# Optimization experiments

Measured on AMD Instinct MI355X. Metric: run time of the kernel, lower is better.

Reference implementation:

```python
import jax, jax.numpy as jnp
import numpy as np

D_MODEL = 768
N_HEAD = 12


def setup_inputs() -> dict:
    key = jax.random.key(0)
    k1, k2, k3, k4, k5 = jax.random.split(key, 5)
    B, T, C = 4, 2048, D_MODEL
    s = 1.0 / np.sqrt(C)
    return {
        "x": jax.random.normal(k1, (B, T, C), dtype=jnp.float32),
        "w_attn": jax.random.normal(k2, (C, 3 * C), dtype=jnp.float32) * s,
        "b_attn": jax.random.normal(k3, (3 * C,), dtype=jnp.float32) * 0.02,
        "w_proj": jax.random.normal(k4, (C, C), dtype=jnp.float32) * s,
        "b_proj": jax.random.normal(k5, (C,), dtype=jnp.float32) * 0.02,
    }


def reference(x, w_attn, b_attn, w_proj, b_proj):
    B, T, C = x.shape
    H = N_HEAD
    Dh = C // H
    qkv = x @ w_attn + b_attn                      # [B, T, 3C]
    q, k, v = jnp.split(qkv, 3, axis=-1)
    # [B, H, T, Dh]
    q = q.reshape(B, T, H, Dh).transpose(0, 2, 1, 3)
    k = k.reshape(B, T, H, Dh).transpose(0, 2, 1, 3)
    v = v.reshape(B, T, H, Dh).transpose(0, 2, 1, 3)
    att = jnp.einsum("bhqd,bhkd->bhqk", q, k) * (1.0 / np.sqrt(Dh))
    causal = jnp.tril(jnp.ones((T, T), dtype=bool))
    att = jnp.where(causal[None, None, :, :], att, -jnp.inf)
    att = jax.nn.softmax(att, axis=-1)             # dropout p=0 (eval)
    y = jnp.einsum("bhqk,bhkd->bhqd", att, v)      # [B, H, T, Dh]
    y = y.transpose(0, 2, 1, 3).reshape(B, T, C)
    return y @ w_proj + b_proj
```

## Files before the change

### kernel.cpp

```cpp
#include <hip/hip_runtime.h>
#include <stdint.h>

#define NHEAD 12
#define DH 64
#define BATCH 4
#define SEQ 2048
#define CDIM 768
#define MROWS (BATCH*SEQ)

typedef __attribute__((ext_vector_type(8))) short short8;
typedef __attribute__((ext_vector_type(4))) float floatx4;
typedef unsigned int u32;

__device__ inline unsigned short f2bf(float f) {
    union { float f; unsigned u; } v; v.f = f;
    unsigned r = v.u + 0x7FFFu + ((v.u >> 16) & 1u);
    return (unsigned short)(r >> 16);
}

__device__ __forceinline__ u32 pk_bf16(float a, float b) {
    u32 d;
    asm("v_cvt_pk_bf16_f32 %0, %1, %2" : "=v"(d) : "v"(a), "v"(b));
    return d;
}

__device__ __forceinline__ void async_cp16(const unsigned short* g, unsigned short* l) {
    __builtin_amdgcn_global_load_lds(
        (const __attribute__((address_space(1))) u32*)g,
        (__attribute__((address_space(3))) u32*)l, 16, 0, 0);
}

template<int N> __device__ __forceinline__ void waitcnt_vm() {
    if constexpr (N == 0)      asm volatile("s_waitcnt vmcnt(0)" ::: "memory");
    else if constexpr (N == 3) asm volatile("s_waitcnt vmcnt(3)" ::: "memory");
    else if constexpr (N == 4) asm volatile("s_waitcnt vmcnt(4)" ::: "memory");
}

__device__ __forceinline__ void transpose_tile(
    const float* __restrict__ in, unsigned short* __restrict__ out,
    int K, int N, int k0, int n0, unsigned short (*T)[72]) {
    const int t = threadIdx.x;
    const int nc = t & 63, kw = t >> 6;
    for (int i = 0; i < 16; i++) {
        const int kr = kw + i * 4;
        T[nc][kr] = f2bf(in[(size_t)(k0 + kr) * N + n0 + nc]);
    }
    __syncthreads();
    const int row = t >> 2, seg = t & 3;
    uint4 a = *(const uint4*)&T[row][seg * 16];
    uint4 b2 = *(const uint4*)&T[row][seg * 16 + 8];
    unsigned short* o = &out[(size_t)(n0 + row) * K + k0 + seg * 16];
    *(uint4*)o = a;
    *(uint4*)(o + 8) = b2;
}

__global__ __launch_bounds__(256) void prep_kernel(
    const float* __restrict__ x,      unsigned short* __restrict__ xb,
    const float* __restrict__ wa,     unsigned short* __restrict__ wta,
    const float* __restrict__ wp,     unsigned short* __restrict__ wtp) {
    __shared__ unsigned short T[64][72];
    const int lin = blockIdx.x;
    if (lin < 6144) {
        const int i = (lin * 256 + threadIdx.x) * 4;
        float4 f = *(const float4*)(x + i);
        union { unsigned short s[4]; uint2 u; } p;
        p.s[0] = f2bf(f.x); p.s[1] = f2bf(f.y);
        p.s[2] = f2bf(f.z); p.s[3] = f2bf(f.w);
        *(uint2*)(xb + i) = p.u;
    } else if (lin < 6144 + 432) {
        const int t2 = lin - 6144;
        transpose_tile(wa, wta, CDIM, 3 * CDIM, (t2 % 12) * 64, (t2 / 12) * 64, T);
    } else {
        const int t3 = lin - 6576;
        transpose_tile(wp, wtp, CDIM, CDIM, (t3 % 12) * 64, (t3 / 12) * 64, T);
    }
}

template<int MODE, int KD, int BM, int BN>
__global__ __launch_bounds__(256) void gemm_bf16(
    const unsigned short* __restrict__ A,
    const unsigned short* __restrict__ BT,
    const float* __restrict__ bias,
    float* __restrict__ Cout,
    unsigned short* __restrict__ Qout,
    unsigned short* __restrict__ Kout,
    unsigned short* __restrict__ VTout,
    int Ndim)
{
    constexpr int TM = BM / 32, TN = BN / 32;
    constexpr int CHA = BM / 64, CHB = BN / 64;
    __shared__ unsigned short SH[3 * (BM + BN) * 32];
    auto As = [&](int b3) { return &SH[b3 * BM * 32]; };
    auto Bs = [&](int b3) { return &SH[3 * BM * 32 + b3 * BN * 32]; };

    const int tid  = threadIdx.x;
    const int wave = tid >> 6;
    const int lane = tid & 63;
    const int l16  = lane & 15;
    const int quad = lane >> 4;
    const int wm = wave >> 1, wn = wave & 1;
    const int m0 = blockIdx.x * BM;
    const int n0 = blockIdx.y * BN;

    const int rloc = lane >> 2;
    const int gs   = (((lane & 3) ^ (rloc & 3) ^ ((rloc >> 2) & 3))) * 8;
    const int pg   = ((quad ^ (l16 & 3) ^ ((l16 >> 2) & 3))) * 8;

    floatx4 acc[TM][TN];
    for (int i = 0; i < TM; i++)
        for (int j = 0; j < TN; j++) acc[i][j] = (floatx4)0.0f;

    constexpr int NIT = KD / 32;

    auto stageTo = [&](int s, int buf) {
        const int koff = s * 32;
        for (int ch = 0; ch < CHA; ch++) {
            const int row = wave * CHA * 16 + ch * 16 + rloc;
            async_cp16(&A[(size_t)(m0 + row) * KD + koff + gs],
                       &As(buf)[(wave * CHA + ch) * 512]);
        }
        for (int ch = 0; ch < CHB; ch++) {
            const int row = wave * CHB * 16 + ch * 16 + rloc;
            async_cp16(&BT[(size_t)(n0 + row) * KD + koff + gs],
                       &Bs(buf)[(wave * CHB + ch) * 512]);
        }
    };
    stageTo(0, 0);
    stageTo(1, 1);

    int buf = 0;
    for (int it = 0; it < NIT; it++) {
        if (it < NIT - 1) waitcnt_vm<CHA + CHB>();
        else              waitcnt_vm<0>();
        asm volatile("s_barrier" ::: "memory");
        if (it + 2 < NIT) {
            int b2 = buf + 2; if (b2 >= 3) b2 -= 3;
            stageTo(it + 2, b2);
        }
        short8 a[TM], b[TN];
        for (int i = 0; i < TM; i++)
            a[i] = *(const short8*)&As(buf)[(wm * (BM / 2) + i * 16 + l16) * 32 + pg];
        for (int j = 0; j < TN; j++)
            b[j] = *(const short8*)&Bs(buf)[(wn * (BN / 2) + j * 16 + l16) * 32 + pg];
        for (int i = 0; i < TM; i++)
            for (int j = 0; j < TN; j++)
                acc[i][j] = __builtin_amdgcn_mfma_f32_16x16x32_bf16(
                    a[i], b[j], acc[i][j], 0, 0, 0);
        buf++; if (buf >= 3) buf = 0;
    }

    const float QSCALE = 0.18033688011112042f;

    if (MODE == 1 && (n0 / CDIM) == 2) {
        __syncthreads();
        unsigned short* scr = &SH[wave * (64 * 68)];
        for (int i = 0; i < TM; i++) {
            const int tl = i * 16 + quad * 4;
            for (int j = 0; j < TN; j++) {
                const int dl = j * 16 + l16;
                const float bv = bias[n0 + wn * 64 + j * 16 + l16];
                uint2 u;
                u.x = pk_bf16(acc[i][j][0] + bv, acc[i][j][1] + bv);
                u.y = pk_bf16(acc[i][j][2] + bv, acc[i][j][3] + bv);
                *(uint2*)&scr[dl * 68 + tl] = u;
            }
        }
        const int b_ = m0 >> 11;
        const int tg = (m0 & 2047) + wm * 64;
        const int h  = (n0 - 2 * CDIM + wn * 64) >> 6;
        const size_t rowbase = ((size_t)(b_ * NHEAD + h)) * DH;
        for (int p = 0; p < 8; p++) {
            const int d  = p * 8 + (lane >> 3);
            const int tc = (lane & 7) * 8;
            uint4 v = *(const uint4*)&scr[d * 68 + tc];
            *(uint4*)&VTout[(rowbase + d) * SEQ + tg + tc] = v;
        }
        return;
    }

    for (int i = 0; i < TM; i++) {
        const int mbase = m0 + wm * (BM / 2) + i * 16 + quad * 4;
        for (int j = 0; j < TN; j++) {
            const int ncj  = n0 + wn * (BN / 2) + j * 16;
            const int ncol = ncj + l16;
            const float bv = bias[ncol];
            for (int r = 0; r < 4; r++) {
                const int m = mbase + r;
                const float v = acc[i][j][r] + bv;
                if (MODE == 0) {
                    Cout[(size_t)m * Ndim + ncol] = v;
                } else {
                    const int part = ncj / CDIM;
                    const int c = ncol - part * CDIM;
                    const int hh = c >> 6, d = c & 63;
                    const int b_ = m >> 11, t = m & 2047;
                    const size_t bh = (size_t)(b_ * NHEAD + hh);
                    if (part == 0)
                        Qout[(bh * SEQ + t) * DH + d] = f2bf(v * QSCALE);
                    else
                        Kout[(bh * SEQ + t) * DH + d] = f2bf(v);
                }
            }
        }
    }
}

__global__ __launch_bounds__(256) void attn_kernel(
    const unsigned short* __restrict__ Q,
    const unsigned short* __restrict__ K,
    const unsigned short* __restrict__ VT,
    unsigned short* __restrict__ O)
{
    __shared__ unsigned short Kl[2][2][64 * 32];
    __shared__ unsigned short Vl[2][2][64 * 32];
    __shared__ unsigned short Pl[4][16 * 68];

    const int tid  = threadIdx.x;
    const int wave = tid >> 6;
    const int lane = tid & 63;
    const int l16  = lane & 15;
    const int quad = lane >> 4;

    const int lin = blockIdx.x;
    const int grp = lin >> 3;
    const int xs  = grp & 15;
    const int bh  = ((grp >> 4) << 3) | (lin & 7);
    const int h = bh % NHEAD, b = bh / NHEAD;

    const unsigned short* Qp = Q  + (size_t)bh * SEQ * DH;
    const unsigned short* Kp = K  + (size_t)bh * SEQ * DH;
    const unsigned short* Vp = VT + (size_t)bh * DH * SEQ;

    const int rloc = lane >> 2;
    const int gofsK = ((lane & 3) ^ (rloc & 3) ^ ((rloc >> 2) & 3)) * 8;
    const int pg = ((quad ^ (l16 & 3) ^ ((l16 >> 2) & 3))) * 8;
    const int krow = wave * 16 + rloc;

    for (int pass = 0; pass < 2; pass++) {
        const int qtile = pass == 0 ? xs : 31 - xs;
        const int qb = qtile * 64;
        const int qw = qb + wave * 16;
        const int nkt = qtile + 1;

        short8 aq[2];
        for (int c = 0; c < 2; c++)
            aq[c] = *(const short8*)&Qp[(size_t)(qw + l16) * DH + c * 32 + quad * 8];

        floatx4 accO[4];
        for (int dt = 0; dt < 4; dt++) accO[dt] = (floatx4)0.0f;
        float lp = 0.0f;

        for (int c = 0; c < 2; c++) {
            async_cp16(&Kp[(size_t)krow * DH + c * 32 + gofsK],
                       &Kl[0][c][wave * 512]);
            async_cp16(&Vp[(size_t)krow * SEQ + 0 + c * 32 + gofsK],
                       &Vl[0][c][wave * 512]);
        }

        for (int kt = 0; kt < nkt; kt++) {
            const int kb  = kt * 64;
            const int cur = kt & 1;

            asm volatile("s_waitcnt vmcnt(0)" ::: "memory");
            asm volatile("s_barrier" ::: "memory");

            if (kt + 1 < nkt) {
                const int kbn = kb + 64;
                for (int c = 0; c < 2; c++) {
                    async_cp16(&Kp[(size_t)(kbn + krow) * DH + c * 32 + gofsK],
                               &Kl[cur ^ 1][c][wave * 512]);
                    async_cp16(&Vp[(size_t)krow * SEQ + kbn + c * 32 + gofsK],
                               &Vl[cur ^ 1][c][wave * 512]);
                }
            }

            floatx4 s[4];
            for (int jn = 0; jn < 4; jn++) {
                s[jn] = (floatx4)0.0f;
                for (int c = 0; c < 2; c++) {
                    short8 bk = *(const short8*)
                        &Kl[cur][c][(jn * 16 + l16) * 32 + pg];
                    s[jn] = __builtin_amdgcn_mfma_f32_16x16x32_bf16(
                        bk, aq[c], s[jn], 0, 0, 0);
                }
            }

            if (kt == nkt - 1) {
                const int q = qw + l16;
                for (int jn = 0; jn < 4; jn++) {
                    const int key = kb + jn * 16 + quad * 4;
                    for (int r = 0; r < 4; r++)
                        if (key + r > q) s[jn][r] = -1e30f;
                }
            }

            for (int jn = 0; jn < 4; jn++)
                for (int r = 0; r < 4; r++) {
                    float p = exp2f(s[jn][r]);
                    s[jn][r] = p;
                    lp += p;
                }

            for (int jn = 0; jn < 4; jn++) {
                uint2 u;
                u.x = pk_bf16(s[jn][0], s[jn][1]);
                u.y = pk_bf16(s[jn][2], s[jn][3]);
                *(uint2*)&Pl[wave][l16 * 68 + jn * 16 + quad * 4] = u;
            }
            short8 ap[2];
            for (int c = 0; c < 2; c++) {
                union { short8 v; uint2 u2[2]; } a_;
                const int base = l16 * 68 + c * 32 + quad * 8;
                a_.u2[0] = *(const uint2*)&Pl[wave][base];
                a_.u2[1] = *(const uint2*)&Pl[wave][base + 4];
                ap[c] = a_.v;
            }

            for (int dt = 0; dt < 4; dt++)
                for (int c = 0; c < 2; c++) {
                    short8 bv = *(const short8*)
                        &Vl[cur][c][(dt * 16 + l16) * 32 + pg];
                    accO[dt] = __builtin_amdgcn_mfma_f32_16x16x32_bf16(
                        ap[c], bv, accO[dt], 0, 0, 0);
                }
        }

        float L = lp;
        L += __shfl_xor(L, 16);
        L += __shfl_xor(L, 32);
        for (int r = 0; r < 4; r++) {
            const float Lr = __shfl(L, (lane & 48) | (quad * 4 + r), 64);
            const float inv = 1.0f / Lr;
            const int t = qb + wave * 16 + quad * 4 + r;
            const size_t base = ((size_t)b * SEQ + t) * CDIM + h * DH;
            for (int dt = 0; dt < 4; dt++)
                O[base + dt * 16 + l16] = f2bf(accO[dt][r] * inv);
        }
        __syncthreads();
    }
}

extern "C" void kernel_launch(void* const* d_in, const int* in_sizes, int n_in,
                              void* d_out, int out_size, void* d_ws, size_t ws_size,
                              hipStream_t stream) {
    const float* x      = (const float*)d_in[0];
    const float* w_attn = (const float*)d_in[1];
    const float* b_attn = (const float*)d_in[2];
    const float* w_proj = (const float*)d_in[3];
    const float* b_proj = (const float*)d_in[4];
    float* out = (float*)d_out;

    unsigned short* xb   = (unsigned short*)d_ws;
    unsigned short* wta  = xb  + (size_t)MROWS * CDIM;
    unsigned short* wtp  = wta + (size_t)3 * CDIM * CDIM;
    unsigned short* qws  = wtp + (size_t)CDIM * CDIM;
    unsigned short* kws  = qws + (size_t)MROWS * CDIM;
    unsigned short* vtws = kws + (size_t)MROWS * CDIM;
    unsigned short* ob   = xb;

    prep_kernel<<<6720, 256, 0, stream>>>(x, xb, w_attn, wta, w_proj, wtp);

    dim3 g1(MROWS / 128, (3 * CDIM) / 128);
    gemm_bf16<1, CDIM, 128, 128><<<g1, 256, 0, stream>>>(
        xb, wta, b_attn, nullptr, qws, kws, vtws, 3 * CDIM);

    attn_kernel<<<768, 256, 0, stream>>>(qws, kws, vtws, ob);

    dim3 g3(MROWS / 64, CDIM / 128);
    gemm_bf16<0, CDIM, 64, 128><<<g3, 256, 0, stream>>>(
        ob, wtp, b_proj, out, nullptr, nullptr, nullptr, CDIM);
}
```

Baseline: 210.8 us.

## Use two waves per attention block, each handling 32 query rows

The attention kernel now runs 128 threads (2 waves) per block instead of 4. Each wave processes two 16-row query sub-tiles, so every K and V fragment read from shared memory feeds two MFMAs. This cuts LDS reads per unit of compute and halves the barrier participants. In exchange each wave holds more registers (two sets of accumulators and Q fragments), does more per-thread async copy work, and each block has fewer waves to hide latency.

After: 225.7 us. 7.0% more time.

```diff
diff --git a/kernel.cpp b/kernel.cpp
--- a/kernel.cpp
+++ b/kernel.cpp
@@ -205,7 +205,7 @@
     }
 }
 
-__global__ __launch_bounds__(256) void attn_kernel(
+__global__ __launch_bounds__(128) void attn_kernel(
     const unsigned short* __restrict__ Q,
     const unsigned short* __restrict__ K,
     const unsigned short* __restrict__ VT,
@@ -213,7 +213,7 @@
 {
     __shared__ unsigned short Kl[2][2][64 * 32];
     __shared__ unsigned short Vl[2][2][64 * 32];
-    __shared__ unsigned short Pl[4][16 * 68];
+    __shared__ unsigned short Pl[2][32 * 68];
 
     const int tid  = threadIdx.x;
     const int wave = tid >> 6;
@@ -232,30 +232,33 @@
     const unsigned short* Vp = VT + (size_t)bh * DH * SEQ;
 
     const int rloc = lane >> 2;
-    const int gofsK = ((lane & 3) ^ (rloc & 3) ^ ((rloc >> 2) & 3)) * 8;
-    const int pg = ((quad ^ (l16 & 3) ^ ((l16 >> 2) & 3))) * 8;
-    const int krow = wave * 16 + rloc;
+    const int gofs = ((lane & 3) ^ (rloc & 3) ^ ((rloc >> 2) & 3)) * 8;
+    const int pg   = ((quad ^ (l16 & 3) ^ ((l16 >> 2) & 3))) * 8;
 
     for (int pass = 0; pass < 2; pass++) {
         const int qtile = pass == 0 ? xs : 31 - xs;
         const int qb = qtile * 64;
-        const int qw = qb + wave * 16;
         const int nkt = qtile + 1;
 
-        short8 aq[2];
+        short8 aq[2][2];
+        for (int qi = 0; qi < 2; qi++)
+            for (int c = 0; c < 2; c++)
+                aq[qi][c] = *(const short8*)
+                    &Qp[(size_t)(qb + wave * 32 + qi * 16 + l16) * DH + c * 32 + quad * 8];
+
+        floatx4 accO[2][4];
+        for (int qi = 0; qi < 2; qi++)
+            for (int dt = 0; dt < 4; dt++) accO[qi][dt] = (floatx4)0.0f;
+        float lp[2] = {0.f, 0.f};
+
         for (int c = 0; c < 2; c++)
-            aq[c] = *(const short8*)&Qp[(size_t)(qw + l16) * DH + c * 32 + quad * 8];
-
-        floatx4 accO[4];
-        for (int dt = 0; dt < 4; dt++) accO[dt] = (floatx4)0.0f;
-        float lp = 0.0f;
-
-        for (int c = 0; c < 2; c++) {
-            async_cp16(&Kp[(size_t)krow * DH + c * 32 + gofsK],
-                       &Kl[0][c][wave * 512]);
-            async_cp16(&Vp[(size_t)krow * SEQ + 0 + c * 32 + gofsK],
-                       &Vl[0][c][wave * 512]);
-        }
+            for (int ch = 0; ch < 2; ch++) {
+                const int row = wave * 32 + ch * 16 + rloc;
+                async_cp16(&Kp[(size_t)row * DH + c * 32 + gofs],
+                           &Kl[0][c][(wave * 2 + ch) * 512]);
+                async_cp16(&Vp[(size_t)row * SEQ + 0 + c * 32 + gofs],
+                           &Vl[0][c][(wave * 2 + ch) * 512]);
+            }
 
         for (int kt = 0; kt < nkt; kt++) {
             const int kb  = kt * 64;
@@ -266,75 +269,87 @@
 
             if (kt + 1 < nkt) {
                 const int kbn = kb + 64;
+                for (int c = 0; c < 2; c++)
+                    for (int ch = 0; ch < 2; ch++) {
+                        const int row = wave * 32 + ch * 16 + rloc;
+                        async_cp16(&Kp[(size_t)(kbn + row) * DH + c * 32 + gofs],
+                                   &Kl[cur ^ 1][c][(wave * 2 + ch) * 512]);
+                        async_cp16(&Vp[(size_t)row * SEQ + kbn + c * 32 + gofs],
+                                   &Vl[cur ^ 1][c][(wave * 2 + ch) * 512]);
+                    }
+            }
+
+            floatx4 s[2][4];
+            for (int jn = 0; jn < 4; jn++) {
+                short8 bk0 = *(const short8*)&Kl[cur][0][(jn * 16 + l16) * 32 + pg];
+                short8 bk1 = *(const short8*)&Kl[cur][1][(jn * 16 + l16) * 32 + pg];
+                for (int qi = 0; qi < 2; qi++) {
+                    floatx4 t0 = __builtin_amdgcn_mfma_f32_16x16x32_bf16(
+                        bk0, aq[qi][0], (floatx4)0.0f, 0, 0, 0);
+                    s[qi][jn] = __builtin_amdgcn_mfma_f32_16x16x32_bf16(
+                        bk1, aq[qi][1], t0, 0, 0, 0);
+                }
+            }
+
+            if (kt == nkt - 1) {
+                for (int qi = 0; qi < 2; qi++) {
+                    const int q = qb + wave * 32 + qi * 16 + l16;
+                    for (int jn = 0; jn < 4; jn++) {
+                        const int key = kb + jn * 16 + quad * 4;
+                        for (int r = 0; r < 4; r++)
+                            if (key + r > q) s[qi][jn][r] = -1e30f;
+                    }
+                }
+            }
+
+            for (int qi = 0; qi < 2; qi++) {
+                float sum = lp[qi];
+                for (int jn = 0; jn < 4; jn++)
+                    for (int r = 0; r < 4; r++) {
+                        float p = exp2f(s[qi][jn][r]);
+                        s[qi][jn][r] = p;
+                        sum += p;
+                    }
+                lp[qi] = sum;
+                for (int jn = 0; jn < 4; jn++) {
+                    uint2 u;
+                    u.x = pk_bf16(s[qi][jn][0], s[qi][jn][1]);
+                    u.y = pk_bf16(s[qi][jn][2], s[qi][jn][3]);
+                    *(uint2*)&Pl[wave][(qi * 16 + l16) * 68 + jn * 16 + quad * 4] = u;
+                }
+            }
+            short8 ap[2][2];
+            for (int qi = 0; qi < 2; qi++)
                 for (int c = 0; c < 2; c++) {
-                    async_cp16(&Kp[(size_t)(kbn + krow) * DH + c * 32 + gofsK],
-                               &Kl[cur ^ 1][c][wave * 512]);
-                    async_cp16(&Vp[(size_t)krow * SEQ + kbn + c * 32 + gofsK],
-                               &Vl[cur ^ 1][c][wave * 512]);
-                }
-            }
-
-            floatx4 s[4];
-            for (int jn = 0; jn < 4; jn++) {
-                s[jn] = (floatx4)0.0f;
-                for (int c = 0; c < 2; c++) {
-                    short8 bk = *(const short8*)
-                        &Kl[cur][c][(jn * 16 + l16) * 32 + pg];
-                    s[jn] = __builtin_amdgcn_mfma_f32_16x16x32_bf16(
-                        bk, aq[c], s[jn], 0, 0, 0);
-                }
-            }
-
-            if (kt == nkt - 1) {
-                const int q = qw + l16;
-                for (int jn = 0; jn < 4; jn++) {
-                    const int key = kb + jn * 16 + quad * 4;
-                    for (int r = 0; r < 4; r++)
-                        if (key + r > q) s[jn][r] = -1e30f;
-                }
-            }
-
-            for (int jn = 0; jn < 4; jn++)
-                for (int r = 0; r < 4; r++) {
-                    float p = exp2f(s[jn][r]);
-                    s[jn][r] = p;
-                    lp += p;
-                }
-
-            for (int jn = 0; jn < 4; jn++) {
-                uint2 u;
-                u.x = pk_bf16(s[jn][0], s[jn][1]);
-                u.y = pk_bf16(s[jn][2], s[jn][3]);
-                *(uint2*)&Pl[wave][l16 * 68 + jn * 16 + quad * 4] = u;
-            }
-            short8 ap[2];
-            for (int c = 0; c < 2; c++) {
-                union { short8 v; uint2 u2[2]; } a_;
-                const int base = l16 * 68 + c * 32 + quad * 8;
-                a_.u2[0] = *(const uint2*)&Pl[wave][base];
-                a_.u2[1] = *(const uint2*)&Pl[wave][base + 4];
-                ap[c] = a_.v;
-            }
+                    union { short8 v; uint2 u2[2]; } a_;
+                    const int base = (qi * 16 + l16) * 68 + c * 32 + quad * 8;
+                    a_.u2[0] = *(const uint2*)&Pl[wave][base];
+                    a_.u2[1] = *(const uint2*)&Pl[wave][base + 4];
+                    ap[qi][c] = a_.v;
+                }
 
             for (int dt = 0; dt < 4; dt++)
                 for (int c = 0; c < 2; c++) {
                     short8 bv = *(const short8*)
                         &Vl[cur][c][(dt * 16 + l16) * 32 + pg];
-                    accO[dt] = __builtin_amdgcn_mfma_f32_16x16x32_bf16(
-                        ap[c], bv, accO[dt], 0, 0, 0);
-                }
-        }
-
-        float L = lp;
-        L += __shfl_xor(L, 16);
-        L += __shfl_xor(L, 32);
-        for (int r = 0; r < 4; r++) {
-            const float Lr = __shfl(L, (lane & 48) | (quad * 4 + r), 64);
-            const float inv = 1.0f / Lr;
-            const int t = qb + wave * 16 + quad * 4 + r;
-            const size_t base = ((size_t)b * SEQ + t) * CDIM + h * DH;
-            for (int dt = 0; dt < 4; dt++)
-                O[base + dt * 16 + l16] = f2bf(accO[dt][r] * inv);
+                    for (int qi = 0; qi < 2; qi++)
+                        accO[qi][dt] = __builtin_amdgcn_mfma_f32_16x16x32_bf16(
+                            ap[qi][c], bv, accO[qi][dt], 0, 0, 0);
+                }
+        }
+
+        for (int qi = 0; qi < 2; qi++) {
+            float L = lp[qi];
+            L += __shfl_xor(L, 16);
+            L += __shfl_xor(L, 32);
+            for (int r = 0; r < 4; r++) {
+                const float Lr = __shfl(L, (lane & 48) | (quad * 4 + r), 64);
+                const float inv = 1.0f / Lr;
+                const int t = qb + wave * 32 + qi * 16 + quad * 4 + r;
+                const size_t base = ((size_t)b * SEQ + t) * CDIM + h * DH;
+                for (int dt = 0; dt < 4; dt++)
+                    O[base + dt * 16 + l16] = f2bf(accO[qi][dt][r] * inv);
+            }
         }
         __syncthreads();
     }
@@ -364,7 +379,7 @@
     gemm_bf16<1, CDIM, 128, 128><<<g1, 256, 0, stream>>>(
         xb, wta, b_attn, nullptr, qws, kws, vtws, 3 * CDIM);
 
-    attn_kernel<<<768, 256, 0, stream>>>(qws, kws, vtws, ob);
+    attn_kernel<<<768, 128, 0, stream>>>(qws, kws, vtws, ob);
 
     dim3 g3(MROWS / 64, CDIM / 128);
     gemm_bf16<0, CDIM, 64, 128><<<g3, 256, 0, stream>>>(
```

## Process low and high causal query tiles together in one pass sharing K/V tiles

Applied to the files above, without the earlier changes.

Instead of two sequential passes over K/V for the paired low and high query tiles, the attention kernel now runs a single loop over the high tile's key range. It computes both tiles' scores against the same staged K/V shared-memory tiles, with the low tile masked off once its causal range ends. This removes the duplicate K/V loads and barriers of the first pass and gives more independent MFMA work per iteration, at the cost of more registers (two accumulator sets) and a doubled P scratch buffer.

Result: slower. 215.7 us (+2.3%).

```diff
diff --git a/kernel.cpp b/kernel.cpp
--- a/kernel.cpp
+++ b/kernel.cpp
@@ -213,7 +213,7 @@
 {
     __shared__ unsigned short Kl[2][2][64 * 32];
     __shared__ unsigned short Vl[2][2][64 * 32];
-    __shared__ unsigned short Pl[4][16 * 68];
+    __shared__ unsigned short Pl[4][32 * 68];
 
     const int tid  = threadIdx.x;
     const int wave = tid >> 6;
@@ -232,111 +232,162 @@
     const unsigned short* Vp = VT + (size_t)bh * DH * SEQ;
 
     const int rloc = lane >> 2;
-    const int gofsK = ((lane & 3) ^ (rloc & 3) ^ ((rloc >> 2) & 3)) * 8;
-    const int pg = ((quad ^ (l16 & 3) ^ ((l16 >> 2) & 3))) * 8;
+    const int gofs = ((lane & 3) ^ (rloc & 3) ^ ((rloc >> 2) & 3)) * 8;
+    const int pg   = ((quad ^ (l16 & 3) ^ ((l16 >> 2) & 3))) * 8;
     const int krow = wave * 16 + rloc;
 
-    for (int pass = 0; pass < 2; pass++) {
-        const int qtile = pass == 0 ? xs : 31 - xs;
-        const int qb = qtile * 64;
-        const int qw = qb + wave * 16;
-        const int nkt = qtile + 1;
-
-        short8 aq[2];
-        for (int c = 0; c < 2; c++)
-            aq[c] = *(const short8*)&Qp[(size_t)(qw + l16) * DH + c * 32 + quad * 8];
-
-        floatx4 accO[4];
-        for (int dt = 0; dt < 4; dt++) accO[dt] = (floatx4)0.0f;
-        float lp = 0.0f;
-
-        for (int c = 0; c < 2; c++) {
-            async_cp16(&Kp[(size_t)krow * DH + c * 32 + gofsK],
-                       &Kl[0][c][wave * 512]);
-            async_cp16(&Vp[(size_t)krow * SEQ + 0 + c * 32 + gofsK],
-                       &Vl[0][c][wave * 512]);
-        }
-
-        for (int kt = 0; kt < nkt; kt++) {
-            const int kb  = kt * 64;
-            const int cur = kt & 1;
-
-            asm volatile("s_waitcnt vmcnt(0)" ::: "memory");
-            asm volatile("s_barrier" ::: "memory");
-
-            if (kt + 1 < nkt) {
-                const int kbn = kb + 64;
-                for (int c = 0; c < 2; c++) {
-                    async_cp16(&Kp[(size_t)(kbn + krow) * DH + c * 32 + gofsK],
-                               &Kl[cur ^ 1][c][wave * 512]);
-                    async_cp16(&Vp[(size_t)krow * SEQ + kbn + c * 32 + gofsK],
-                               &Vl[cur ^ 1][c][wave * 512]);
-                }
-            }
-
-            floatx4 s[4];
+    const int qtL = xs, qtH = 31 - xs;
+    const int qbL = qtL * 64, qbH = qtH * 64;
+    const int qwL = qbL + wave * 16, qwH = qbH + wave * 16;
+    const int nkt = qtH + 1;
+
+    short8 aqL[2], aqH[2];
+    for (int c = 0; c < 2; c++) {
+        aqL[c] = *(const short8*)&Qp[(size_t)(qwL + l16) * DH + c * 32 + quad * 8];
+        aqH[c] = *(const short8*)&Qp[(size_t)(qwH + l16) * DH + c * 32 + quad * 8];
+    }
+
+    floatx4 accL[4], accH[4];
+    for (int dt = 0; dt < 4; dt++) { accL[dt] = (floatx4)0.0f; accH[dt] = (floatx4)0.0f; }
+    float lpL = 0.0f, lpH = 0.0f;
+
+    for (int c = 0; c < 2; c++) {
+        async_cp16(&Kp[(size_t)krow * DH + c * 32 + gofs], &Kl[0][c][wave * 512]);
+        async_cp16(&Vp[(size_t)krow * SEQ + 0 + c * 32 + gofs], &Vl[0][c][wave * 512]);
+    }
+
+    for (int kt = 0; kt < nkt; kt++) {
+        const int kb  = kt * 64;
+        const int cur = kt & 1;
+        const bool doL = (kt <= qtL);
+
+        asm volatile("s_waitcnt vmcnt(0)" ::: "memory");
+        asm volatile("s_barrier" ::: "memory");
+
+        if (kt + 1 < nkt) {
+            const int kbn = kb + 64;
+            for (int c = 0; c < 2; c++) {
+                async_cp16(&Kp[(size_t)(kbn + krow) * DH + c * 32 + gofs],
+                           &Kl[cur ^ 1][c][wave * 512]);
+                async_cp16(&Vp[(size_t)krow * SEQ + kbn + c * 32 + gofs],
+                           &Vl[cur ^ 1][c][wave * 512]);
+            }
+        }
+
+        floatx4 sH[4], sL[4];
+        for (int jn = 0; jn < 4; jn++) {
+            short8 bk0 = *(const short8*)&Kl[cur][0][(jn * 16 + l16) * 32 + pg];
+            short8 bk1 = *(const short8*)&Kl[cur][1][(jn * 16 + l16) * 32 + pg];
+            floatx4 t0 = __builtin_amdgcn_mfma_f32_16x16x32_bf16(
+                bk0, aqH[0], (floatx4)0.0f, 0, 0, 0);
+            sH[jn] = __builtin_amdgcn_mfma_f32_16x16x32_bf16(
+                bk1, aqH[1], t0, 0, 0, 0);
+            if (doL) {
+                floatx4 t1 = __builtin_amdgcn_mfma_f32_16x16x32_bf16(
+                    bk0, aqL[0], (floatx4)0.0f, 0, 0, 0);
+                sL[jn] = __builtin_amdgcn_mfma_f32_16x16x32_bf16(
+                    bk1, aqL[1], t1, 0, 0, 0);
+            }
+        }
+
+        if (kt == nkt - 1) {
+            const int q = qwH + l16;
             for (int jn = 0; jn < 4; jn++) {
-                s[jn] = (floatx4)0.0f;
-                for (int c = 0; c < 2; c++) {
-                    short8 bk = *(const short8*)
-                        &Kl[cur][c][(jn * 16 + l16) * 32 + pg];
-                    s[jn] = __builtin_amdgcn_mfma_f32_16x16x32_bf16(
-                        bk, aq[c], s[jn], 0, 0, 0);
-                }
-            }
-
-            if (kt == nkt - 1) {
-                const int q = qw + l16;
-                for (int jn = 0; jn < 4; jn++) {
-                    const int key = kb + jn * 16 + quad * 4;
-                    for (int r = 0; r < 4; r++)
-                        if (key + r > q) s[jn][r] = -1e30f;
-                }
-            }
-
+                const int key = kb + jn * 16 + quad * 4;
+                for (int r = 0; r < 4; r++)
+                    if (key + r > q) sH[jn][r] = -1e30f;
+            }
+        }
+        if (doL && kt == qtL) {
+            const int q = qwL + l16;
+            for (int jn = 0; jn < 4; jn++) {
+                const int key = kb + jn * 16 + quad * 4;
+                for (int r = 0; r < 4; r++)
+                    if (key + r > q) sL[jn][r] = -1e30f;
+            }
+        }
+
+        for (int jn = 0; jn < 4; jn++)
+            for (int r = 0; r < 4; r++) {
+                float p = exp2f(sH[jn][r]);
+                sH[jn][r] = p;
+                lpH += p;
+            }
+        for (int jn = 0; jn < 4; jn++) {
+            uint2 u;
+            u.x = pk_bf16(sH[jn][0], sH[jn][1]);
+            u.y = pk_bf16(sH[jn][2], sH[jn][3]);
+            *(uint2*)&Pl[wave][(16 + l16) * 68 + jn * 16 + quad * 4] = u;
+        }
+        if (doL) {
             for (int jn = 0; jn < 4; jn++)
                 for (int r = 0; r < 4; r++) {
-                    float p = exp2f(s[jn][r]);
-                    s[jn][r] = p;
-                    lp += p;
+                    float p = exp2f(sL[jn][r]);
+                    sL[jn][r] = p;
+                    lpL += p;
                 }
-
             for (int jn = 0; jn < 4; jn++) {
                 uint2 u;
-                u.x = pk_bf16(s[jn][0], s[jn][1]);
-                u.y = pk_bf16(s[jn][2], s[jn][3]);
+                u.x = pk_bf16(sL[jn][0], sL[jn][1]);
+                u.y = pk_bf16(sL[jn][2], sL[jn][3]);
                 *(uint2*)&Pl[wave][l16 * 68 + jn * 16 + quad * 4] = u;
             }
-            short8 ap[2];
+        }
+
+        short8 apH[2], apL[2];
+        for (int c = 0; c < 2; c++) {
+            union { short8 v; uint2 u2[2]; } a_;
+            const int baseH = (16 + l16) * 68 + c * 32 + quad * 8;
+            a_.u2[0] = *(const uint2*)&Pl[wave][baseH];
+            a_.u2[1] = *(const uint2*)&Pl[wave][baseH + 4];
+            apH[c] = a_.v;
+        }
+        if (doL)
             for (int c = 0; c < 2; c++) {
                 union { short8 v; uint2 u2[2]; } a_;
-                const int base = l16 * 68 + c * 32 + quad * 8;
-                a_.u2[0] = *(const uint2*)&Pl[wave][base];
-                a_.u2[1] = *(const uint2*)&Pl[wave][base + 4];
-                ap[c] = a_.v;
-            }
-
-            for (int dt = 0; dt < 4; dt++)
-                for (int c = 0; c < 2; c++) {
-                    short8 bv = *(const short8*)
-                        &Vl[cur][c][(dt * 16 + l16) * 32 + pg];
-                    accO[dt] = __builtin_amdgcn_mfma_f32_16x16x32_bf16(
-                        ap[c], bv, accO[dt], 0, 0, 0);
-                }
-        }
-
-        float L = lp;
+                const int baseL = l16 * 68 + c * 32 + quad * 8;
+                a_.u2[0] = *(const uint2*)&Pl[wave][baseL];
+                a_.u2[1] = *(const uint2*)&Pl[wave][baseL + 4];
+                apL[c] = a_.v;
+            }
+
+        for (int dt = 0; dt < 4; dt++)
+            for (int c = 0; c < 2; c++) {
+                short8 bv = *(const short8*)
+                    &Vl[cur][c][(dt * 16 + l16) * 32 + pg];
+                accH[dt] = __builtin_amdgcn_mfma_f32_16x16x32_bf16(
+                    apH[c], bv, accH[dt], 0, 0, 0);
+                if (doL)
+                    accL[dt] = __builtin_amdgcn_mfma_f32_16x16x32_bf16(
+                        apL[c], bv, accL[dt], 0, 0, 0);
+            }
+    }
+
+    {
+        float L = lpL;
         L += __shfl_xor(L, 16);
         L += __shfl_xor(L, 32);
         for (int r = 0; r < 4; r++) {
             const float Lr = __shfl(L, (lane & 48) | (quad * 4 + r), 64);
             const float inv = 1.0f / Lr;
-            const int t = qb + wave * 16 + quad * 4 + r;
+            const int t = qbL + wave * 16 + quad * 4 + r;
             const size_t base = ((size_t)b * SEQ + t) * CDIM + h * DH;
             for (int dt = 0; dt < 4; dt++)
-                O[base + dt * 16 + l16] = f2bf(accO[dt][r] * inv);
-        }
-        __syncthreads();
+                O[base + dt * 16 + l16] = f2bf(accL[dt][r] * inv);
+        }
+    }
+    {
+        float L = lpH;
+        L += __shfl_xor(L, 16);
+        L += __shfl_xor(L, 32);
+        for (int r = 0; r < 4; r++) {
+            const float Lr = __shfl(L, (lane & 48) | (quad * 4 + r), 64);
+            const float inv = 1.0f / Lr;
+            const int t = qbH + wave * 16 + quad * 4 + r;
+            const size_t base = ((size_t)b * SEQ + t) * CDIM + h * DH;
+            for (int dt = 0; dt < 4; dt++)
+                O[base + dt * 16 + l16] = f2bf(accH[dt][r] * inv);
+        }
     }
 }
 
```
